# Optimization experiments

Measured on AMD Instinct MI355X. Metric: run time of the kernel, lower is better.

The kernel has to match this reference:

```python
import math
import jax, jax.numpy as jnp
import numpy as np

H = 16  # num_heads
B, L, D = 1, 256, 1024


def setup_inputs() -> dict:
    key = jax.random.key(0)
    ks = jax.random.split(key, 12)
    s = 1.0 / math.sqrt(D)  # keep activations O(1)
    inp = {
        "mu": jax.random.normal(ks[0], (B, L, D), jnp.float32),
        "var": jax.random.uniform(ks[1], (B, L, D), jnp.float32) + 0.1,
    }
    names = ["q_mu", "q_var", "k_mu", "k_var", "v_mu", "v_var", "o_mu", "o_var"]
    for i, n in enumerate(names):
        inp["w" + n] = jax.random.normal(ks[2 + i], (D, D), jnp.float32) * s
        inp["b" + n] = jnp.zeros((D,), jnp.float32)
    return inp


def _split_heads(x):
    b, l, d = x.shape
    return x.reshape(b, l, H, d // H).transpose(0, 2, 1, 3)  # [B,H,L,Dh]


def _combine_heads(x):
    b, h, l, dh = x.shape
    return x.transpose(0, 2, 1, 3).reshape(b, l, h * dh)


def reference(mu, var, wq_mu, bq_mu, wq_var, bq_var, wk_mu, bk_mu, wk_var, bk_var,
              wv_mu, bv_mu, wv_var, bv_var, wo_mu, bo_mu, wo_var, bo_var):
    dk = mu.shape[-1] // H
    Qm = _split_heads(mu @ wq_mu + bq_mu)
    Qv = _split_heads(jax.nn.softplus(var @ wq_var + bq_var))
    Km = _split_heads(mu @ wk_mu + bk_mu)
    Kv = _split_heads(jax.nn.softplus(var @ wk_var + bk_var))
    Vm = _split_heads(mu @ wv_mu + bv_mu)
    Vv = _split_heads(jax.nn.softplus(var @ wv_var + bv_var))

    # per-element Gaussian KL, broadcast to [B,H,Lq,Lk,Dh] (as in the original)
    diff = (Qm[:, :, :, None, :] - Km[:, :, None, :, :]) ** 2
    ratio = Qv[:, :, :, None, :] / Kv[:, :, None, :, :]
    kl = diff / (2.0 * Kv[:, :, None, :, :]) + 0.5 * (ratio - jnp.log(ratio) - 1.0)
    scores = -kl.sum(-1) * (1.0 / math.sqrt(dk))  # [B,H,Lq,Lk]
    attn = jax.nn.softmax(scores, axis=-1)

    out_mu = jnp.einsum("bhqk,bhkd->bhqd", attn, Vm)
    out_var = jnp.einsum("bhqk,bhkd->bhqd", attn ** 2, Vv)

    O_mu = _combine_heads(out_mu)
    O_var = _combine_heads(out_var)
    mu_out = O_mu @ wo_mu + bo_mu
    var_out = jax.nn.softplus(O_var @ wo_var + bo_var)
    return mu_out, var_out
```

## Files before the change

### kernel.cpp

```cpp
#include <hip/hip_runtime.h>
#include <math.h>

typedef __bf16 bf16_t;
typedef bf16_t bf16x4 __attribute__((ext_vector_type(4)));
typedef bf16_t bf16x8 __attribute__((ext_vector_type(8)));
typedef float  f32x4  __attribute__((ext_vector_type(4)));

__device__ __forceinline__ float softplus_f(float x) {
    return (x > 20.f) ? x : log1pf(expf(x));
}

__device__ __forceinline__ float fast_rcp(float x) {
#if __has_builtin(__builtin_amdgcn_rcpf)
    return __builtin_amdgcn_rcpf(x);
#else
    return 1.0f / x;
#endif
}

template<bool AF32>
__device__ __forceinline__ void gemmT_core(const void* Aptr, const float* __restrict__ Wf,
                                           const int m_base, const int n_base,
                                           unsigned char* smem, const int t, f32x4 out[4]) {
    __syncthreads();
    bf16_t* stage = (bf16_t*)smem;
    float*  Cr    = (float*)smem;
    const int lane = t & 63, w = t >> 6;
    bf16_t* As = stage + w * 9216;
    bf16_t* Bs = As + 4608;
    const int r8 = lane >> 3, kb = lane & 7;
    const int fr = lane & 15, fq = lane >> 4, fk = fq * 8;
    const int bc = fr;
    const int br16 = fq * 16;

    const float*  Af = (const float*)Aptr  + (size_t)m_base * 1024 + w * 256 + kb * 8;
    const bf16_t* Ab = (const bf16_t*)Aptr + (size_t)m_base * 1024 + w * 256 + kb * 8;
    const float*  Bf = Wf + (size_t)(w * 256 + br16) * 1024 + n_base + bc * 4;

    f32x4 acc[4][4] = {};
    bf16x8 pa[8];
    f32x4 paf0[8], paf1[8];
    f32x4 pbf[16];

#pragma unroll
    for (int i = 0; i < 8; ++i) {
        if constexpr (AF32) {
            paf0[i] = *(const f32x4*)(Af + (size_t)(i * 8 + r8) * 1024);
            paf1[i] = *(const f32x4*)(Af + (size_t)(i * 8 + r8) * 1024 + 4);
        } else {
            pa[i] = *(const bf16x8*)(Ab + (size_t)(i * 8 + r8) * 1024);
        }
    }
#pragma unroll
    for (int i = 0; i < 16; ++i)
        pbf[i] = *(const f32x4*)(Bf + (size_t)i * 1024);

#pragma unroll
    for (int s = 0; s < 4; ++s) {
#pragma unroll
        for (int i = 0; i < 8; ++i) {
            bf16x8 av;
            if constexpr (AF32) {
#pragma unroll
                for (int e = 0; e < 4; ++e) {
                    av[e]     = (bf16_t)paf0[i][e];
                    av[e + 4] = (bf16_t)paf1[i][e];
                }
            } else {
                av = pa[i];
            }
            *(bf16x8*)&As[(i * 8 + r8) * 72 + kb * 8] = av;
        }
#pragma unroll
        for (int e = 0; e < 4; ++e) {
            bf16x8 lo, hi;
#pragma unroll
            for (int q = 0; q < 8; ++q) {
                lo[q] = (bf16_t)pbf[q][e];
                hi[q] = (bf16_t)pbf[q + 8][e];
            }
            *(bf16x8*)&Bs[(bc * 4 + e) * 72 + br16]     = lo;
            *(bf16x8*)&Bs[(bc * 4 + e) * 72 + br16 + 8] = hi;
        }
        if (s < 3) {
            const int off = (s + 1) * 64;
#pragma unroll
            for (int i = 0; i < 8; ++i) {
                if constexpr (AF32) {
                    paf0[i] = *(const f32x4*)(Af + (size_t)(i * 8 + r8) * 1024 + off);
                    paf1[i] = *(const f32x4*)(Af + (size_t)(i * 8 + r8) * 1024 + off + 4);
                } else {
                    pa[i] = *(const bf16x8*)(Ab + (size_t)(i * 8 + r8) * 1024 + off);
                }
            }
#pragma unroll
            for (int i = 0; i < 16; ++i)
                pbf[i] = *(const f32x4*)(Bf + (size_t)i * 1024 + (size_t)off * 1024);
        }
#pragma unroll
        for (int kh = 0; kh < 2; ++kh) {
            bf16x8 aF[4], bF[4];
#pragma unroll
            for (int i = 0; i < 4; ++i)
                aF[i] = *(const bf16x8*)&As[(i * 16 + fr) * 72 + kh * 32 + fk];
#pragma unroll
            for (int j = 0; j < 4; ++j)
                bF[j] = *(const bf16x8*)&Bs[(j * 16 + fr) * 72 + kh * 32 + fk];
#pragma unroll
            for (int i = 0; i < 4; ++i)
#pragma unroll
                for (int j = 0; j < 4; ++j)
                    acc[i][j] = __builtin_amdgcn_mfma_f32_16x16x32_bf16(aF[i], bF[j], acc[i][j], 0, 0, 0);
        }
    }

    __syncthreads();
    {
        float* Crw = Cr + w * 4352;
        const int orow = fq * 4;
#pragma unroll
        for (int i = 0; i < 4; ++i)
#pragma unroll
            for (int j = 0; j < 4; ++j)
#pragma unroll
                for (int rr = 0; rr < 4; ++rr)
                    Crw[(i * 16 + orow + rr) * 68 + j * 16 + fr] = acc[i][j][rr];
    }
    __syncthreads();

    const int cc = (t & 15) * 4;
#pragma unroll
    for (int i = 0; i < 4; ++i) {
        const int row = (t >> 4) + i * 16;
        f32x4 s0 = *(const f32x4*)&Cr[0 * 4352 + row * 68 + cc];
        f32x4 s1 = *(const f32x4*)&Cr[1 * 4352 + row * 68 + cc];
        f32x4 s2 = *(const f32x4*)&Cr[2 * 4352 + row * 68 + cc];
        f32x4 s3 = *(const f32x4*)&Cr[3 * 4352 + row * 68 + cc];
        out[i] = (s0 + s1) + (s2 + s3);
    }
}

struct ProjArgs {
    const float* mu; const float* var;
    const float* W[6];
    const float* bias[6];
    float* Proj;
    bf16_t* Gbf; float* cvec;
};

__global__ __launch_bounds__(256, 2) void proj_kernel(ProjArgs a) {
    __shared__ __align__(16) unsigned char smem[73728];
    const int z = blockIdx.z;
    const int nb = blockIdx.x * 64, mb = blockIdx.y * 64;
    const int t = threadIdx.x;
    const int cc = (t & 15) * 4;

    if (z != 2) {
        const int wi   = (z < 2) ? z : (z + 1);
        const int slot = (z < 2) ? z : (z - 1);
        const int sp   = (z == 1) || (z == 4);
        const void* A  = (z == 1 || z == 4) ? (const void*)a.var : (const void*)a.mu;
        f32x4 o[4];
        gemmT_core<true>(A, a.W[wi], mb, nb, smem, t, o);
        const f32x4 bv = *(const f32x4*)&a.bias[wi][nb + cc];
        float* dst = a.Proj + (size_t)slot * 262144;
#pragma unroll
        for (int i = 0; i < 4; ++i) {
            const int row = (t >> 4) + i * 16;
            f32x4 v = o[i] + bv;
            if (sp) {
                v[0] = softplus_f(v[0]); v[1] = softplus_f(v[1]);
                v[2] = softplus_f(v[2]); v[3] = softplus_f(v[3]);
            }
            *(f32x4*)&dst[(size_t)(mb + row) * 1024 + nb + cc] = v;
        }
    } else {
        const int h = blockIdx.x;
        f32x4 okm[4], okv[4];
        gemmT_core<true>(a.mu,  a.W[2], mb, nb, smem, t, okm);
        gemmT_core<true>(a.var, a.W[3], mb, nb, smem, t, okv);
        const f32x4 bkm = *(const f32x4*)&a.bias[2][nb + cc];
        const f32x4 bkv = *(const f32x4*)&a.bias[3][nb + cc];
#pragma unroll
        for (int i = 0; i < 4; ++i) {
            const int row = (t >> 4) + i * 16;
            const int katt = mb + row;
            const f32x4 km  = okm[i] + bkm;
            const f32x4 kvr = okv[i] + bkv;
            bf16x4 o1, o2;
            float c = 0.f;
#pragma unroll
            for (int e = 0; e < 4; ++e) {
                const float kv = softplus_f(kvr[e]);
                const float r  = 0.5f * fast_rcp(kv);
                o1[e] = (bf16_t)r;
                o2[e] = (bf16_t)(-2.f * km[e] * r);
                c += km[e] * km[e] * r + 0.5f * __logf(kv);
            }
            bf16_t* grow = a.Gbf + ((size_t)(h * 256 + katt)) * 128;
            *(bf16x4*)&grow[cc]      = o1;
            *(bf16x4*)&grow[64 + cc] = o2;
#pragma unroll
            for (int off = 8; off > 0; off >>= 1)
                c += __shfl_xor(c, off, 16);
            if ((t & 15) == 0)
                a.cvec[h * 256 + katt] = c;
        }
    }
}

#define OFF_VM   0
#define OFF_VV   36864
#define OFF_FS   73728
#define OFF_SC   82176
#define OFF_PHI  98816
#define OFF_PLO  107264
#define OFF_P2H  115712
#define OFF_P2L  124160
#define ATTN_SMEM 132608

__global__ __launch_bounds__(512) void attn_v7(const float* __restrict__ Qm,
                                               const float* __restrict__ Qv,
                                               const bf16_t* __restrict__ Gbf,
                                               const float* __restrict__ cvec,
                                               const float* __restrict__ Vm,
                                               const float* __restrict__ Vv,
                                               bf16_t* __restrict__ Omu,
                                               bf16_t* __restrict__ Ovar) {
    __shared__ __align__(16) unsigned char smem[ATTN_SMEM];
    bf16_t* Vsm = (bf16_t*)(smem + OFF_VM);
    bf16_t* Vsv = (bf16_t*)(smem + OFF_VV);
    float*  Fs  = (float*)(smem + OFF_FS);
    float*  Sc  = (float*)(smem + OFF_SC);
    bf16_t* Phi = (bf16_t*)(smem + OFF_PHI);
    bf16_t* Plo = (bf16_t*)(smem + OFF_PLO);
    bf16_t* P2h = (bf16_t*)(smem + OFF_P2H);
    bf16_t* P2l = (bf16_t*)(smem + OFF_P2L);

    const int qt = blockIdx.x, h = blockIdx.y;
    const int t = threadIdx.x, w = t >> 6, lane = t & 63;
    const int fr = lane & 15, fq = lane >> 4;
    const int n0 = w * 32;

    const bf16_t* gB = Gbf + ((size_t)(h * 256 + n0 + fr)) * 128 + fq * 8;

    bf16x8 bcur[4];
#pragma unroll
    for (int ks = 0; ks < 4; ++ks) bcur[ks] = *(const bf16x8*)(gB + ks * 32);

    if (t < 256) {
        const int r = t >> 4, c = t & 15;
        f32x4 qm = *(const f32x4*)(Qm + (size_t)(qt * 16 + r) * 1024 + h * 64 + c * 4);
        f32x4 qv = *(const f32x4*)(Qv + (size_t)(qt * 16 + r) * 1024 + h * 64 + c * 4);
        *(f32x4*)&Fs[r * 132 + c * 4]      = qm * qm + qv;
        *(f32x4*)&Fs[r * 132 + 64 + c * 4] = qm;
    }
    __syncthreads();

    bf16x8 ahi[4], alo[4];
#pragma unroll
    for (int ks = 0; ks < 4; ++ks) {
        f32x4 f0 = *(const f32x4*)&Fs[fr * 132 + ks * 32 + fq * 8];
        f32x4 f1 = *(const f32x4*)&Fs[fr * 132 + ks * 32 + fq * 8 + 4];
#pragma unroll
        for (int e = 0; e < 4; ++e) {
            bf16_t hb = (bf16_t)f0[e];
            ahi[ks][e] = hb; alo[ks][e] = (bf16_t)(f0[e] - (float)hb);
            bf16_t hb2 = (bf16_t)f1[e];
            ahi[ks][e + 4] = hb2; alo[ks][e + 4] = (bf16_t)(f1[e] - (float)hb2);
        }
    }

    const int tm = t & 255;
    const int vk = tm >> 2, vpart = tm & 3;
    const float* Vsrc = (t >= 256) ? Vv : Vm;
    bf16_t*      Vdst = (t >= 256) ? Vsv : Vsm;

#pragma unroll
    for (int nt = 0; nt < 2; ++nt) {
        const int ra = vk + (2 * nt) * 64;
        const int rb = vk + (2 * nt + 1) * 64;
        const float* vsa = Vsrc + (size_t)ra * 1024 + h * 64 + vpart * 16;
        const float* vsb = Vsrc + (size_t)rb * 1024 + h * 64 + vpart * 16;
        f32x4 va0 = *(const f32x4*)(vsa),     va1 = *(const f32x4*)(vsa + 4);
        f32x4 va2 = *(const f32x4*)(vsa + 8), va3 = *(const f32x4*)(vsa + 12);
        f32x4 vb0 = *(const f32x4*)(vsb),     vb1 = *(const f32x4*)(vsb + 4);
        f32x4 vb2 = *(const f32x4*)(vsb + 8), vb3 = *(const f32x4*)(vsb + 12);

        bf16x8 bnxt[4];
        if (nt < 1) {
#pragma unroll
            for (int ks = 0; ks < 4; ++ks)
                bnxt[ks] = *(const bf16x8*)(gB + 2048 + ks * 32);
        }

        f32x4 acc = {0.f, 0.f, 0.f, 0.f};
#pragma unroll
        for (int ks = 0; ks < 4; ++ks) {
            acc = __builtin_amdgcn_mfma_f32_16x16x32_bf16(ahi[ks], bcur[ks], acc, 0, 0, 0);
            acc = __builtin_amdgcn_mfma_f32_16x16x32_bf16(alo[ks], bcur[ks], acc, 0, 0, 0);
        }

        {
            bf16_t* da = Vdst + ra * 72 + vpart * 16;
            bf16_t* db = Vdst + rb * 72 + vpart * 16;
            bf16x8 o0, o1;
            o0[0]=(bf16_t)va0[0]; o0[1]=(bf16_t)va0[1]; o0[2]=(bf16_t)va0[2]; o0[3]=(bf16_t)va0[3];
            o0[4]=(bf16_t)va1[0]; o0[5]=(bf16_t)va1[1]; o0[6]=(bf16_t)va1[2]; o0[7]=(bf16_t)va1[3];
            o1[0]=(bf16_t)va2[0]; o1[1]=(bf16_t)va2[1]; o1[2]=(bf16_t)va2[2]; o1[3]=(bf16_t)va2[3];
            o1[4]=(bf16_t)va3[0]; o1[5]=(bf16_t)va3[1]; o1[6]=(bf16_t)va3[2]; o1[7]=(bf16_t)va3[3];
            *(bf16x8*)(da)     = o0;
            *(bf16x8*)(da + 8) = o1;
            o0[0]=(bf16_t)vb0[0]; o0[1]=(bf16_t)vb0[1]; o0[2]=(bf16_t)vb0[2]; o0[3]=(bf16_t)vb0[3];
            o0[4]=(bf16_t)vb1[0]; o0[5]=(bf16_t)vb1[1]; o0[6]=(bf16_t)vb1[2]; o0[7]=(bf16_t)vb1[3];
            o1[0]=(bf16_t)vb2[0]; o1[1]=(bf16_t)vb2[1]; o1[2]=(bf16_t)vb2[2]; o1[3]=(bf16_t)vb2[3];
            o1[4]=(bf16_t)vb3[0]; o1[5]=(bf16_t)vb3[1]; o1[6]=(bf16_t)vb3[2]; o1[7]=(bf16_t)vb3[3];
            *(bf16x8*)(db)     = o0;
            *(bf16x8*)(db + 8) = o1;
        }

        const float cv = cvec[h * 256 + n0 + nt * 16 + fr];
        f32x4 lg = (acc + cv) * (-0.125f);
#pragma unroll
        for (int reg = 0; reg < 4; ++reg)
            Sc[(fq * 4 + reg) * 260 + n0 + nt * 16 + fr] = lg[reg];

#pragma unroll
        for (int ks = 0; ks < 4; ++ks) bcur[ks] = bnxt[ks];
    }
    __syncthreads();

    const int fw = w * 2;
    f32x4 sr[2];
#pragma unroll
    for (int r = 0; r < 2; ++r)
        sr[r] = *(const f32x4*)&Sc[(fw + r) * 260 + lane * 4];
#pragma unroll
    for (int r = 0; r < 2; ++r) {
        f32x4 s = sr[r];
        float mloc = fmaxf(fmaxf(s[0], s[1]), fmaxf(s[2], s[3]));
#pragma unroll
        for (int off = 32; off > 0; off >>= 1)
            mloc = fmaxf(mloc, __shfl_xor(mloc, off, 64));
        s[0] = __expf(s[0] - mloc); s[1] = __expf(s[1] - mloc);
        s[2] = __expf(s[2] - mloc); s[3] = __expf(s[3] - mloc);
        float sl = (s[0] + s[1]) + (s[2] + s[3]);
#pragma unroll
        for (int off = 32; off > 0; off >>= 1)
            sl += __shfl_xor(sl, off, 64);
        sr[r] = s * fast_rcp(sl);
    }

#pragma unroll
    for (int r = 0; r < 2; ++r) {
        bf16x4 phi, plo, p2hi, p2lo;
#pragma unroll
        for (int e = 0; e < 4; ++e) {
            const float p = sr[r][e];
            const bf16_t hb = (bf16_t)p;
            phi[e] = hb; plo[e] = (bf16_t)(p - (float)hb);
            const float p2 = p * p;
            const bf16_t h2 = (bf16_t)p2;
            p2hi[e] = h2; p2lo[e] = (bf16_t)(p2 - (float)h2);
        }
        const int row = fw + r;
        *(bf16x4*)&Phi[row * 264 + lane * 4] = phi;
        *(bf16x4*)&Plo[row * 264 + lane * 4] = plo;
        *(bf16x4*)&P2h[row * 264 + lane * 4] = p2hi;
        *(bf16x4*)&P2l[row * 264 + lane * 4] = p2lo;
    }
    __syncthreads();

    const int tile = w & 3;
    const int isvar = w >> 2;
    const bf16_t* Pa = isvar ? P2h : Phi;
    const bf16_t* Pb = isvar ? P2l : Plo;
    const bf16_t* Vs = isvar ? Vsv : Vsm;
    f32x4 accp = {0.f, 0.f, 0.f, 0.f};
#pragma unroll
    for (int k0 = 0; k0 < 256; k0 += 32) {
        const int ka = k0 + fq * 8;
        bf16x8 a1 = *(const bf16x8*)&Pa[fr * 264 + ka];
        bf16x8 a2 = *(const bf16x8*)&Pb[fr * 264 + ka];
        bf16x8 bfr;
#pragma unroll
        for (int j = 0; j < 8; ++j)
            bfr[j] = Vs[(ka + j) * 72 + tile * 16 + fr];
        accp = __builtin_amdgcn_mfma_f32_16x16x32_bf16(a1, bfr, accp, 0, 0, 0);
        accp = __builtin_amdgcn_mfma_f32_16x16x32_bf16(a2, bfr, accp, 0, 0, 0);
    }

    bf16_t* Out = isvar ? Ovar : Omu;
#pragma unroll
    for (int reg = 0; reg < 4; ++reg) {
        const int qg = qt * 16 + fq * 4 + reg;
        const size_t ob = (size_t)qg * 1024 + h * 64 + tile * 16 + fr;
        Out[ob] = (bf16_t)accp[reg];
    }
}

struct OutArgs {
    const bf16_t* A[2];
    const float*  W[2];
    const float*  bias[2];
    float*        dst[2];
    int           splus[2];
};

__global__ __launch_bounds__(256, 2) void out_gemm(OutArgs args) {
    const int z = blockIdx.z;
    const bf16_t* __restrict__ A    = args.A[z];
    const float*  __restrict__ W    = args.W[z];
    const float*  __restrict__ bias = args.bias[z];
    float*        __restrict__ dst  = args.dst[z];
    const int sp = args.splus[z];

    const int n_base = blockIdx.x * 64;
    const int m_base = blockIdx.y * 64;

    __shared__ __align__(16) unsigned char smem[73728];
    const int t = threadIdx.x;
    f32x4 o[4];
    gemmT_core<false>(A, W, m_base, n_base, smem, t, o);

    const int cc = (t & 15) * 4;
    const f32x4 bv = *(const f32x4*)&bias[n_base + cc];
#pragma unroll
    for (int i = 0; i < 4; ++i) {
        const int row = (t >> 4) + i * 16;
        f32x4 v = o[i] + bv;
        if (sp) {
            v[0] = softplus_f(v[0]); v[1] = softplus_f(v[1]);
            v[2] = softplus_f(v[2]); v[3] = softplus_f(v[3]);
        }
        *(f32x4*)&dst[(size_t)(m_base + row) * 1024 + n_base + cc] = v;
    }
}

extern "C" void kernel_launch(void* const* d_in, const int* in_sizes, int n_in,
                              void* d_out, int out_size, void* d_ws, size_t ws_size,
                              hipStream_t stream) {
    const float* mu  = (const float*)d_in[0];
    const float* var = (const float*)d_in[1];
    uint8_t* ws = (uint8_t*)d_ws;

    float*  Proj = (float*)(ws);
    bf16_t* Obm  = (bf16_t*)(ws + (4u << 20));
    bf16_t* Obv  = (bf16_t*)(ws + (4u << 20) + (512u << 10));
    bf16_t* Gbf  = (bf16_t*)(ws + (5u << 20));
    float*  cvec = (float*)(ws + (6u << 20));

    ProjArgs pr;
    pr.mu = mu; pr.var = var;
    for (int i = 0; i < 6; ++i) {
        pr.W[i]    = (const float*)d_in[2 + 2 * i];
        pr.bias[i] = (const float*)d_in[3 + 2 * i];
    }
    pr.Proj = Proj; pr.Gbf = Gbf; pr.cvec = cvec;
    proj_kernel<<<dim3(16, 4, 5), 256, 0, stream>>>(pr);

    attn_v7<<<dim3(16, 16), 512, 0, stream>>>(Proj, Proj + 262144, Gbf, cvec,
                                              Proj + 2 * 262144, Proj + 3 * 262144,
                                              Obm, Obv);

    OutArgs g3;
    g3.A[0] = Obm;  g3.W[0] = (const float*)d_in[14];
    g3.bias[0] = (const float*)d_in[15];
    g3.dst[0] = (float*)d_out;             g3.splus[0] = 0;
    g3.A[1] = Obv;  g3.W[1] = (const float*)d_in[16];
    g3.bias[1] = (const float*)d_in[17];
    g3.dst[1] = (float*)d_out + 262144;    g3.splus[1] = 1;
    out_gemm<<<dim3(16, 4, 2), 256, 0, stream>>>(g3);
}
```

Before: 148.5 us.

## Linearize grids with XCD-aware block mapping and split fused K-projection blocks

All three launches now use a 1D grid. Block indices are remapped so that consecutive groups of 8 blocks, which the hardware spreads across the 8 XCDs, share weight columns or heads. This is meant to improve L2 locality. The fused K-mean/K-var projection blocks, which ran two GEMMs each and dominated the tail, are split into twice as many 32-row tiles through a new MT template parameter on the GEMM core. This balances per-block work but adds index math and assumes the hidden cvec epilogue still matches the 2-tile layout.

```diff
diff --git a/kernel.cpp b/kernel.cpp
--- a/kernel.cpp
+++ b/kernel.cpp
@@ -18,10 +18,11 @@
 #endif
 }
 
-template<bool AF32>
+template<bool AF32, int MT>
 __device__ __forceinline__ void gemmT_core(const void* Aptr, const float* __restrict__ Wf,
                                            const int m_base, const int n_base,
-                                           unsigned char* smem, const int t, f32x4 out[4]) {
+                                           unsigned char* smem, const int t, f32x4* out) {
+    constexpr int NA = 2 * MT;
     __syncthreads();
     bf16_t* stage = (bf16_t*)smem;
     float*  Cr    = (float*)smem;
@@ -37,13 +38,13 @@
     const bf16_t* Ab = (const bf16_t*)Aptr + (size_t)m_base * 1024 + w * 256 + kb * 8;
     const float*  Bf = Wf + (size_t)(w * 256 + br16) * 1024 + n_base + bc * 4;
 
-    f32x4 acc[4][4] = {};
-    bf16x8 pa[8];
-    f32x4 paf0[8], paf1[8];
+    f32x4 acc[MT][4] = {};
+    bf16x8 pa[NA];
+    f32x4 paf0[NA], paf1[NA];
     f32x4 pbf[16];
 
 #pragma unroll
-    for (int i = 0; i < 8; ++i) {
+    for (int i = 0; i < NA; ++i) {
         if constexpr (AF32) {
             paf0[i] = *(const f32x4*)(Af + (size_t)(i * 8 + r8) * 1024);
             paf1[i] = *(const f32x4*)(Af + (size_t)(i * 8 + r8) * 1024 + 4);
@@ -58,7 +59,7 @@
 #pragma unroll
     for (int s = 0; s < 4; ++s) {
 #pragma unroll
-        for (int i = 0; i < 8; ++i) {
+        for (int i = 0; i < NA; ++i) {
             bf16x8 av;
             if constexpr (AF32) {
 #pragma unroll
@@ -85,7 +86,7 @@
         if (s < 3) {
             const int off = (s + 1) * 64;
 #pragma unroll
-            for (int i = 0; i < 8; ++i) {
+            for (int i = 0; i < NA; ++i) {
                 if constexpr (AF32) {
                     paf0[i] = *(const f32x4*)(Af + (size_t)(i * 8 + r8) * 1024 + off);
                     paf1[i] = *(const f32x4*)(Af + (size_t)(i * 8 + r8) * 1024 + off + 4);
@@ -99,15 +100,15 @@
         }
 #pragma unroll
         for (int kh = 0; kh < 2; ++kh) {
-            bf16x8 aF[4], bF[4];
-#pragma unroll
-            for (int i = 0; i < 4; ++i)
+            bf16x8 aF[MT], bF[4];
+#pragma unroll
+            for (int i = 0; i < MT; ++i)
                 aF[i] = *(const bf16x8*)&As[(i * 16 + fr) * 72 + kh * 32 + fk];
 #pragma unroll
             for (int j = 0; j < 4; ++j)
                 bF[j] = *(const bf16x8*)&Bs[(j * 16 + fr) * 72 + kh * 32 + fk];
 #pragma unroll
-            for (int i = 0; i < 4; ++i)
+            for (int i = 0; i < MT; ++i)
 #pragma unroll
                 for (int j = 0; j < 4; ++j)
                     acc[i][j] = __builtin_amdgcn_mfma_f32_16x16x32_bf16(aF[i], bF[j], acc[i][j], 0, 0, 0);
@@ -119,7 +120,7 @@
         float* Crw = Cr + w * 4352;
         const int orow = fq * 4;
 #pragma unroll
-        for (int i = 0; i < 4; ++i)
+        for (int i = 0; i < MT; ++i)
 #pragma unroll
             for (int j = 0; j < 4; ++j)
 #pragma unroll
@@ -130,7 +131,7 @@
 
     const int cc = (t & 15) * 4;
 #pragma unroll
-    for (int i = 0; i < 4; ++i) {
+    for (int i = 0; i < MT; ++i) {
         const int row = (t >> 4) + i * 16;
         f32x4 s0 = *(const f32x4*)&Cr[0 * 4352 + row * 68 + cc];
         f32x4 s1 = *(const f32x4*)&Cr[1 * 4352 + row * 68 + cc];
@@ -150,24 +151,29 @@
 
 __global__ __launch_bounds__(256, 2) void proj_kernel(ProjArgs a) {
     __shared__ __align__(16) unsigned char smem[73728];
-    const int z = blockIdx.z;
-    const int nb = blockIdx.x * 64, mb = blockIdx.y * 64;
     const int t = threadIdx.x;
     const int cc = (t & 15) * 4;
-
-    if (z != 2) {
-        const int wi   = (z < 2) ? z : (z + 1);
-        const int slot = (z < 2) ? z : (z - 1);
-        const int sp   = (z == 1) || (z == 4);
-        const void* A  = (z == 1 || z == 4) ? (const void*)a.var : (const void*)a.mu;
-        f32x4 o[4];
-        gemmT_core<true>(A, a.W[wi], mb, nb, smem, t, o);
+    const int L = blockIdx.x;
+    const int x = L & 7;
+    const int o = L >> 3;
+
+    if (o < 32) {
+        const int gA = (o >> 2) * 8 + x;
+        const int m  = o & 3;
+        const int zp = gA >> 4;
+        const int nb = (gA & 15) * 64;
+        const int mb = m * 64;
+        const int wi = (zp < 2) ? zp : (zp + 2);
+        const int sp = (zp == 1) || (zp == 3);
+        const void* A = sp ? (const void*)a.var : (const void*)a.mu;
+        f32x4 ov[4];
+        gemmT_core<true, 4>(A, a.W[wi], mb, nb, smem, t, ov);
         const f32x4 bv = *(const f32x4*)&a.bias[wi][nb + cc];
-        float* dst = a.Proj + (size_t)slot * 262144;
+        float* dst = a.Proj + (size_t)zp * 262144;
 #pragma unroll
         for (int i = 0; i < 4; ++i) {
             const int row = (t >> 4) + i * 16;
-            f32x4 v = o[i] + bv;
+            f32x4 v = ov[i] + bv;
             if (sp) {
                 v[0] = softplus_f(v[0]); v[1] = softplus_f(v[1]);
                 v[2] = softplus_f(v[2]); v[3] = softplus_f(v[3]);
@@ -175,14 +181,18 @@
             *(f32x4*)&dst[(size_t)(mb + row) * 1024 + nb + cc] = v;
         }
     } else {
-        const int h = blockIdx.x;
-        f32x4 okm[4], okv[4];
-        gemmT_core<true>(a.mu,  a.W[2], mb, nb, smem, t, okm);
-        gemmT_core<true>(a.var, a.W[3], mb, nb, smem, t, okv);
+        const int op = o - 32;
+        const int h  = (op >> 3) * 8 + x;
+        const int m  = op & 7;
+        const int mb = m * 32;
+        const int nb = h * 64;
+        f32x4 okm[2], okv[2];
+        gemmT_core<true, 2>(a.mu,  a.W[2], mb, nb, smem, t, okm);
+        gemmT_core<true, 2>(a.var, a.W[3], mb, nb, smem, t, okv);
         const f32x4 bkm = *(const f32x4*)&a.bias[2][nb + cc];
         const f32x4 bkv = *(const f32x4*)&a.bias[3][nb + cc];
 #pragma unroll
-        for (int i = 0; i < 4; ++i) {
+        for (int i = 0; i < 2; ++i) {
             const int row = (t >> 4) + i * 16;
             const int katt = mb + row;
             const f32x4 km  = okm[i] + bkm;
@@ -237,7 +247,10 @@
     bf16_t* P2h = (bf16_t*)(smem + OFF_P2H);
     bf16_t* P2l = (bf16_t*)(smem + OFF_P2L);
 
-    const int qt = blockIdx.x, h = blockIdx.y;
+    const int L = blockIdx.x;
+    const int h  = ((L >> 7) << 3) + (L & 7);
+    const int qt = (L >> 3) & 15;
+
     const int t = threadIdx.x, w = t >> 6, lane = t & 63;
     const int fr = lane & 15, fq = lane >> 4;
     const int n0 = w * 32;
@@ -408,27 +421,31 @@
 };
 
 __global__ __launch_bounds__(256, 2) void out_gemm(OutArgs args) {
-    const int z = blockIdx.z;
+    __shared__ __align__(16) unsigned char smem[73728];
+    const int t = threadIdx.x;
+    const int L = blockIdx.x;
+    const int x = L & 7, o = L >> 3;
+    const int g = (o >> 2) * 8 + x;
+    const int m = o & 3;
+    const int z = g >> 4;
+    const int n_base = (g & 15) * 64;
+    const int m_base = m * 64;
+
     const bf16_t* __restrict__ A    = args.A[z];
     const float*  __restrict__ W    = args.W[z];
     const float*  __restrict__ bias = args.bias[z];
     float*        __restrict__ dst  = args.dst[z];
     const int sp = args.splus[z];
 
-    const int n_base = blockIdx.x * 64;
-    const int m_base = blockIdx.y * 64;
-
-    __shared__ __align__(16) unsigned char smem[73728];
-    const int t = threadIdx.x;
-    f32x4 o[4];
-    gemmT_core<false>(A, W, m_base, n_base, smem, t, o);
+    f32x4 ov[4];
+    gemmT_core<false, 4>(A, W, m_base, n_base, smem, t, ov);
 
     const int cc = (t & 15) * 4;
     const f32x4 bv = *(const f32x4*)&bias[n_base + cc];
 #pragma unroll
     for (int i = 0; i < 4; ++i) {
         const int row = (t >> 4) + i * 16;
-        f32x4 v = o[i] + bv;
+        f32x4 v = ov[i] + bv;
         if (sp) {
             v[0] = softplus_f(v[0]); v[1] = softplus_f(v[1]);
             v[2] = softplus_f(v[2]); v[3] = softplus_f(v[3]);
@@ -457,11 +474,11 @@
         pr.bias[i] = (const float*)d_in[3 + 2 * i];
     }
     pr.Proj = Proj; pr.Gbf = Gbf; pr.cvec = cvec;
-    proj_kernel<<<dim3(16, 4, 5), 256, 0, stream>>>(pr);
-
-    attn_v7<<<dim3(16, 16), 512, 0, stream>>>(Proj, Proj + 262144, Gbf, cvec,
-                                              Proj + 2 * 262144, Proj + 3 * 262144,
-                                              Obm, Obv);
+    proj_kernel<<<dim3(384), 256, 0, stream>>>(pr);
+
+    attn_v7<<<dim3(256), 512, 0, stream>>>(Proj, Proj + 262144, Gbf, cvec,
+                                           Proj + 2 * 262144, Proj + 3 * 262144,
+                                           Obm, Obv);
 
     OutArgs g3;
     g3.A[0] = Obm;  g3.W[0] = (const float*)d_in[14];
@@ -470,5 +487,5 @@
     g3.A[1] = Obv;  g3.W[1] = (const float*)d_in[16];
     g3.bias[1] = (const float*)d_in[17];
     g3.dst[1] = (float*)d_out + 262144;    g3.splus[1] = 1;
-    out_gemm<<<dim3(16, 4, 2), 256, 0, stream>>>(g3);
-}
+    out_gemm<<<dim3(128), 256, 0, stream>>>(g3);
+}
```

Result: faster. 144.5 us (-2.7%).
